# Kernel optimization log

Hardware: AMD Instinct MI355X
Metric: run time of the kernel (lower is better)

## Reference

```python
import jax, jax.numpy as jnp
import numpy as np

B, POOL, PACK = 4096, 45, 15
E, D, V = 512, 8, 30000  # embedding_dim, internal_dims, num_cards
SQRT_D = float(np.sqrt(D))


def setup_inputs() -> dict:
    key = jax.random.key(0)
    ks = jax.random.split(key, 12)
    s = 0.02
    return {
        "pool": jax.random.randint(ks[0], (B, POOL), 0, V),
        "pack": jax.random.randint(ks[1], (B, PACK), 0, V),
        "wins": jax.random.uniform(ks[2], (B,), dtype=jnp.float32),
        "ranks": jax.random.uniform(ks[3], (B,), dtype=jnp.float32),
        "emb_table": jax.random.normal(ks[4], (V, E), dtype=jnp.float32) * s,
        "win_w": jax.random.normal(ks[5], (E, 1), dtype=jnp.float32) * s,
        "win_b": jnp.zeros((E,), dtype=jnp.float32),
        "rank_w": jax.random.normal(ks[6], (E, 1), dtype=jnp.float32) * s,
        "rank_b": jnp.zeros((E,), dtype=jnp.float32),
        "q_w": jax.random.normal(ks[7], (D, E), dtype=jnp.float32) * s,
        "k_w": jax.random.normal(ks[8], (D, E), dtype=jnp.float32) * s,
        "v_w": jax.random.normal(ks[9], (D, E), dtype=jnp.float32) * s,
        "sc_w": jax.random.normal(ks[10], (1, D), dtype=jnp.float32) * s,
        "sc_b": jnp.zeros((1,), dtype=jnp.float32),
    }


def reference(pool, pack, wins, ranks, emb_table, win_w, win_b,
              rank_w, rank_b, q_w, k_w, v_w, sc_w, sc_b):
    pool_emb = emb_table[pool]                                   # [B, POOL, E]
    pack_emb = emb_table[pack]                                   # [B, PACK, E]
    win_emb = wins[:, None, None] * win_w[:, 0] + win_b          # [B, 1, E]
    rank_emb = ranks[:, None, None] * rank_w[:, 0] + rank_b      # [B, 1, E]
    pool_full = jnp.concatenate([pool_emb, win_emb, rank_emb], axis=1)  # [B, POOL+2, E]
    pool_full = jax.nn.relu(pool_full)
    q = jnp.einsum("bke,de->bkd", pack_emb, q_w)                 # [B, PACK, D]
    k = jnp.einsum("bpe,de->bpd", pool_full, k_w)                # [B, POOL+2, D]
    v = jnp.einsum("bpe,de->bpd", pool_full, v_w)                # [B, POOL+2, D]
    scores = jnp.einsum("bkd,bpd->bkp", q, k) / SQRT_D
    attn = jax.nn.softmax(jax.nn.relu(scores), axis=-1)          # [B, PACK, POOL+2]
    context = jnp.einsum("bkp,bpd->bkd", attn, v)                # [B, PACK, D]
    context = jax.nn.leaky_relu(context, negative_slope=0.01)
    logits = jnp.einsum("bkd,od->bko", context, sc_w) + sc_b     # [B, PACK, 1]
    return logits[..., 0]                                        # [B, PACK]
```

## Files before the change

kernel.cpp:

```cpp
#include <hip/hip_runtime.h>

#define B_N 4096
#define POOL_N 45
#define PACK_N 15
#define E_N 512
#define D_N 8
#define V_N 30000

#define WT_SZ  (E_N * 24)
#define TAB_SZ (V_N * 24)
#define AUX_SZ (B_N * 32)

__global__ __launch_bounds__(256) void k_transpose_w(const float* __restrict__ q_w,
                                                     const float* __restrict__ k_w,
                                                     const float* __restrict__ v_w,
                                                     float* __restrict__ wt) {
  int i = blockIdx.x * 256 + threadIdx.x;
  if (i >= E_N * 24) return;
  int e = i / 24, j = i % 24;
  float val = (j < 8) ? q_w[j * E_N + e]
            : (j < 16) ? k_w[(j - 8) * E_N + e]
                       : v_w[(j - 16) * E_N + e];
  wt[i] = val;
}

__global__ __launch_bounds__(256) void k_build_tab(const float* __restrict__ emb,
                                                   const float* __restrict__ wt,
                                                   float* __restrict__ tab) {
  __shared__ float lds[128 * 65];
  int t = threadIdx.x;
  int lane = t & 63;
  int w = __builtin_amdgcn_readfirstlane(t >> 6);
  int row0 = blockIdx.x * 64;
  int f4 = t & 31;
  int sr0 = t >> 5;
  float acc[24];
#pragma unroll
  for (int j = 0; j < 24; ++j) acc[j] = 0.f;

  for (int it = 0; it < 4; ++it) {
    int eb = it * 128;
    __syncthreads();
#pragma unroll
    for (int sub = 0; sub < 8; ++sub) {
      int sr = sub * 8 + sr0;
      int gr = row0 + sr;
      if (gr > V_N - 1) gr = V_N - 1;
      float4 v = *(const float4*)(emb + (size_t)gr * E_N + eb + f4 * 4);
      float* d = lds + (f4 * 4) * 65 + sr;
      d[0] = v.x; d[65] = v.y; d[130] = v.z; d[195] = v.w;
    }
    __syncthreads();
    const float* wp = wt + (size_t)(eb + w * 32) * 24;
    const float* ep = lds + (w * 32) * 65 + lane;
#pragma unroll
    for (int el = 0; el < 32; ++el) {
      float x = ep[el * 65];
      float xr = fmaxf(x, 0.f);
      const float* wr = wp + el * 24;
#pragma unroll
      for (int j = 0; j < 8; ++j) acc[j] = fmaf(x, wr[j], acc[j]);
#pragma unroll
      for (int j = 8; j < 24; ++j) acc[j] = fmaf(xr, wr[j], acc[j]);
    }
  }
  __syncthreads();
#pragma unroll
  for (int j = 0; j < 24; ++j) lds[w * 1600 + lane * 25 + j] = acc[j];
  __syncthreads();
  for (int o = t; o < 1536; o += 256) {
    int row = o / 24, col = o - row * 24;
    int r_out = row0 + row;
    if (r_out < V_N) {
      float v = lds[row * 25 + col] + lds[1600 + row * 25 + col]
              + lds[3200 + row * 25 + col] + lds[4800 + row * 25 + col];
      tab[(size_t)r_out * 24 + col] = v;
    }
  }
}

__global__ __launch_bounds__(256) void k_build_aux(const float* __restrict__ wins,
                                                   const float* __restrict__ ranks,
                                                   const float* __restrict__ win_w,
                                                   const float* __restrict__ win_b,
                                                   const float* __restrict__ rank_w,
                                                   const float* __restrict__ rank_b,
                                                   const float* __restrict__ wt,
                                                   float* __restrict__ aux) {
  __shared__ float red[16][16][17];
  int t = threadIdx.x;
  int bl = t & 15, seg = t >> 4;
  int which = blockIdx.y;
  int b = blockIdx.x * 16 + bl;
  float s = which ? ranks[b] : wins[b];
  const float* ww = which ? rank_w : win_w;
  const float* wb = which ? rank_b : win_b;
  float acc[16];
#pragma unroll
  for (int j = 0; j < 16; ++j) acc[j] = 0.f;
  int e0 = seg * 32;
#pragma unroll 4
  for (int e = e0; e < e0 + 32; ++e) {
    float x = fmaf(s, ww[e], wb[e]);
    float xr = fmaxf(x, 0.f);
    const float* wr = wt + e * 24 + 8;
#pragma unroll
    for (int j = 0; j < 16; ++j) acc[j] = fmaf(xr, wr[j], acc[j]);
  }
#pragma unroll
  for (int j = 0; j < 16; ++j) red[seg][bl][j] = acc[j];
  __syncthreads();
  int bi = t >> 4, j = t & 15;
  float v = 0.f;
#pragma unroll
  for (int sg = 0; sg < 16; ++sg) v += red[sg][bi][j];
  aux[(size_t)(blockIdx.x * 16 + bi) * 32 + which * 16 + j] = v;
}

__global__ __launch_bounds__(256) void k_main(const int* __restrict__ pool,
                                              const int* __restrict__ pack,
                                              const float* __restrict__ tab,
                                              const float* __restrict__ aux,
                                              const float* __restrict__ sc_w,
                                              const float* __restrict__ sc_b,
                                              float* __restrict__ out) {
  int grp = threadIdx.x >> 5;
  int lane = threadIdx.x & 31;
  int b = blockIdx.x * 8 + grp;
  int i0 = pool[(size_t)b * POOL_N + lane];
  int i1 = (lane < POOL_N - 32) ? pool[(size_t)b * POOL_N + 32 + lane] : 0;
  int k = (lane < PACK_N) ? lane : 0;
  int qidx = pack[(size_t)b * PACK_N + k];
  const float* qr = tab + (size_t)qidx * 24;
  float4 qa = *(const float4*)qr;
  float4 qb = *(const float4*)(qr + 4);
  const float rs = 0.35355339059327373f;
  const float* auxb = aux + (size_t)b * 32;

  float m = 0.f, sum = 0.f;
  float ctx[8] = {0.f, 0.f, 0.f, 0.f, 0.f, 0.f, 0.f, 0.f};

  auto att_step = [&](const float* kr) {
    float4 k0 = *(const float4*)kr;
    float4 k1 = *(const float4*)(kr + 4);
    float4 v0 = *(const float4*)(kr + 8);
    float4 v1 = *(const float4*)(kr + 12);
    float d = qa.x * k0.x;
    d = fmaf(qa.y, k0.y, d);
    d = fmaf(qa.z, k0.z, d);
    d = fmaf(qa.w, k0.w, d);
    d = fmaf(qb.x, k1.x, d);
    d = fmaf(qb.y, k1.y, d);
    d = fmaf(qb.z, k1.z, d);
    d = fmaf(qb.w, k1.w, d);
    d = fmaxf(d * rs, 0.f);
    float t = __expf(-fabsf(d - m));
    bool up = d > m;
    float sc = up ? t : 1.f;
    float e = up ? 1.f : t;
    m = fmaxf(m, d);
    sum = fmaf(sum, sc, e);
    ctx[0] = fmaf(ctx[0], sc, e * v0.x);
    ctx[1] = fmaf(ctx[1], sc, e * v0.y);
    ctx[2] = fmaf(ctx[2], sc, e * v0.z);
    ctx[3] = fmaf(ctx[3], sc, e * v0.w);
    ctx[4] = fmaf(ctx[4], sc, e * v1.x);
    ctx[5] = fmaf(ctx[5], sc, e * v1.y);
    ctx[6] = fmaf(ctx[6], sc, e * v1.z);
    ctx[7] = fmaf(ctx[7], sc, e * v1.w);
  };

#pragma unroll 8
  for (int p = 0; p < 32; ++p) {
    int pi = __shfl(i0, p, 32);
    att_step(tab + (size_t)pi * 24 + 8);
  }
#pragma unroll
  for (int p = 0; p < 13; ++p) {
    int pi = __shfl(i1, p, 32);
    att_step(tab + (size_t)pi * 24 + 8);
  }
  att_step(auxb);
  att_step(auxb + 16);

  float inv = 1.f / sum;
  float logit = 0.f;
#pragma unroll
  for (int d0 = 0; d0 < 8; ++d0) {
    float c = ctx[d0] * inv;
    c = (c > 0.f) ? c : 0.01f * c;
    logit = fmaf(c, sc_w[d0], logit);
  }
  logit += sc_b[0];
  if (lane < PACK_N) out[(size_t)b * PACK_N + lane] = logit;
}

extern "C" void kernel_launch(void* const* d_in, const int* in_sizes, int n_in,
                              void* d_out, int out_size, void* d_ws, size_t ws_size,
                              hipStream_t stream) {
  const int* pool = (const int*)d_in[0];
  const int* pack = (const int*)d_in[1];
  const float* wins = (const float*)d_in[2];
  const float* ranks = (const float*)d_in[3];
  const float* emb = (const float*)d_in[4];
  const float* win_w = (const float*)d_in[5];
  const float* win_b = (const float*)d_in[6];
  const float* rank_w = (const float*)d_in[7];
  const float* rank_b = (const float*)d_in[8];
  const float* q_w = (const float*)d_in[9];
  const float* k_w = (const float*)d_in[10];
  const float* v_w = (const float*)d_in[11];
  const float* sc_w = (const float*)d_in[12];
  const float* sc_b = (const float*)d_in[13];

  float* ws = (float*)d_ws;
  float* wt = ws;
  float* tab = ws + WT_SZ;
  float* aux = ws + WT_SZ + TAB_SZ;
  float* out = (float*)d_out;

  hipLaunchKernelGGL(k_transpose_w, dim3(48), dim3(256), 0, stream,
                     q_w, k_w, v_w, wt);
  hipLaunchKernelGGL(k_build_tab, dim3((V_N + 63) / 64), dim3(256), 0, stream,
                     emb, wt, tab);
  hipLaunchKernelGGL(k_build_aux, dim3(B_N / 16, 2), dim3(256), 0, stream,
                     wins, ranks, win_w, win_b, rank_w, rank_b, wt, aux);
  hipLaunchKernelGGL(k_main, dim3(B_N / 8), dim3(256), 0, stream,
                     pool, pack, tab, aux, sc_w, sc_b, out);
}
```

Measured before the change: 61.23 us.

## Double-buffer embedding tiles in build_tab with register prefetch and 512-thread blocks

Restructures the table-build kernel so the next 128-column chunk of embedding rows is loaded into registers while the current chunk is multiplied from LDS. A two-buffer LDS layout with XOR swizzling replaces the padded single buffer. The block grows to 8 waves, each covering 16 features, and the final reduction sums 8 partial accumulators. The goal is to hide global load latency and cut a barrier per chunk. The cost is 64KB of LDS per block, which may limit occupancy.

Measured after the change: 55.23 us. -9.8%, faster.

```diff
diff --git a/kernel.cpp b/kernel.cpp
--- a/kernel.cpp
+++ b/kernel.cpp
@@ -24,56 +24,89 @@
   wt[i] = val;
 }
 
-__global__ __launch_bounds__(256) void k_build_tab(const float* __restrict__ emb,
+__global__ __launch_bounds__(512) void k_build_tab(const float* __restrict__ emb,
                                                    const float* __restrict__ wt,
                                                    float* __restrict__ tab) {
-  __shared__ float lds[128 * 65];
+  __shared__ float lds[2][128 * 64];
   int t = threadIdx.x;
   int lane = t & 63;
   int w = __builtin_amdgcn_readfirstlane(t >> 6);
   int row0 = blockIdx.x * 64;
   int f4 = t & 31;
-  int sr0 = t >> 5;
+  int r0 = t >> 5;
   float acc[24];
 #pragma unroll
   for (int j = 0; j < 24; ++j) acc[j] = 0.f;
 
-  for (int it = 0; it < 4; ++it) {
-    int eb = it * 128;
+  float4 stg[4];
+#pragma unroll
+  for (int s = 0; s < 4; ++s) {
+    int gr = row0 + r0 + s * 16;
+    if (gr >= V_N) gr = V_N - 1;
+    stg[s] = *(const float4*)(emb + (size_t)gr * E_N + f4 * 4);
+  }
+#pragma unroll
+  for (int s = 0; s < 4; ++s) {
+    int row = r0 + s * 16;
+    int e0 = f4 * 4;
+    lds[0][(e0 + 0) * 64 + (row ^ ((e0 + 0) & 63))] = stg[s].x;
+    lds[0][(e0 + 1) * 64 + (row ^ ((e0 + 1) & 63))] = stg[s].y;
+    lds[0][(e0 + 2) * 64 + (row ^ ((e0 + 2) & 63))] = stg[s].z;
+    lds[0][(e0 + 3) * 64 + (row ^ ((e0 + 3) & 63))] = stg[s].w;
+  }
+
+  for (int ch = 0; ch < 4; ++ch) {
     __syncthreads();
-#pragma unroll
-    for (int sub = 0; sub < 8; ++sub) {
-      int sr = sub * 8 + sr0;
-      int gr = row0 + sr;
-      if (gr > V_N - 1) gr = V_N - 1;
-      float4 v = *(const float4*)(emb + (size_t)gr * E_N + eb + f4 * 4);
-      float* d = lds + (f4 * 4) * 65 + sr;
-      d[0] = v.x; d[65] = v.y; d[130] = v.z; d[195] = v.w;
-    }
-    __syncthreads();
-    const float* wp = wt + (size_t)(eb + w * 32) * 24;
-    const float* ep = lds + (w * 32) * 65 + lane;
-#pragma unroll
-    for (int el = 0; el < 32; ++el) {
-      float x = ep[el * 65];
-      float xr = fmaxf(x, 0.f);
-      const float* wr = wp + el * 24;
-#pragma unroll
-      for (int j = 0; j < 8; ++j) acc[j] = fmaf(x, wr[j], acc[j]);
-#pragma unroll
-      for (int j = 8; j < 24; ++j) acc[j] = fmaf(xr, wr[j], acc[j]);
-    }
-  }
+    if (ch < 3) {
+      int eb = (ch + 1) * 128;
+#pragma unroll
+      for (int s = 0; s < 4; ++s) {
+        int gr = row0 + r0 + s * 16;
+        if (gr >= V_N) gr = V_N - 1;
+        stg[s] = *(const float4*)(emb + (size_t)gr * E_N + eb + f4 * 4);
+      }
+    }
+    {
+      const float* wp = wt + (size_t)(ch * 128 + w * 16) * 24;
+      const float* buf = lds[ch & 1];
+#pragma unroll
+      for (int el = 0; el < 16; ++el) {
+        int e_loc = w * 16 + el;
+        float x = buf[e_loc * 64 + (lane ^ (e_loc & 63))];
+        float xr = fmaxf(x, 0.f);
+        const float* wr = wp + el * 24;
+#pragma unroll
+        for (int j = 0; j < 8; ++j) acc[j] = fmaf(x, wr[j], acc[j]);
+#pragma unroll
+        for (int j = 8; j < 24; ++j) acc[j] = fmaf(xr, wr[j], acc[j]);
+      }
+    }
+    if (ch < 3) {
+#pragma unroll
+      for (int s = 0; s < 4; ++s) {
+        int row = r0 + s * 16;
+        int e0 = f4 * 4;
+        float* b = (float*)lds[(ch + 1) & 1];
+        b[(e0 + 0) * 64 + (row ^ ((e0 + 0) & 63))] = stg[s].x;
+        b[(e0 + 1) * 64 + (row ^ ((e0 + 1) & 63))] = stg[s].y;
+        b[(e0 + 2) * 64 + (row ^ ((e0 + 2) & 63))] = stg[s].z;
+        b[(e0 + 3) * 64 + (row ^ ((e0 + 3) & 63))] = stg[s].w;
+      }
+    }
+  }
+
   __syncthreads();
-#pragma unroll
-  for (int j = 0; j < 24; ++j) lds[w * 1600 + lane * 25 + j] = acc[j];
+  float* red = (float*)lds;
+#pragma unroll
+  for (int j = 0; j < 24; ++j) red[w * 1600 + lane * 25 + j] = acc[j];
   __syncthreads();
-  for (int o = t; o < 1536; o += 256) {
+  for (int o = t; o < 1536; o += 512) {
     int row = o / 24, col = o - row * 24;
     int r_out = row0 + row;
     if (r_out < V_N) {
-      float v = lds[row * 25 + col] + lds[1600 + row * 25 + col]
-              + lds[3200 + row * 25 + col] + lds[4800 + row * 25 + col];
+      float v = 0.f;
+#pragma unroll
+      for (int s = 0; s < 8; ++s) v += red[s * 1600 + row * 25 + col];
       tab[(size_t)r_out * 24 + col] = v;
     }
   }
@@ -221,7 +254,7 @@
 
   hipLaunchKernelGGL(k_transpose_w, dim3(48), dim3(256), 0, stream,
                      q_w, k_w, v_w, wt);
-  hipLaunchKernelGGL(k_build_tab, dim3((V_N + 63) / 64), dim3(256), 0, stream,
+  hipLaunchKernelGGL(k_build_tab, dim3((V_N + 63) / 64), dim3(512), 0, stream,
                      emb, wt, tab);
   hipLaunchKernelGGL(k_build_aux, dim3(B_N / 16, 2), dim3(256), 0, stream,
                      wins, ranks, win_w, win_b, rank_w, rank_b, wt, aux);
```
